# Kernel tuning notes

Measured on AMD Instinct MI355X. Metric: run time of the kernel, lower is better.

## Reference

```python
import jax, jax.numpy as jnp
import numpy as np
from jax import lax

B, H, W = 16, 96, 320
NUM_JOINTS = 9
THRESH = 0.1


def _nms(heat):
    # 3x3 max-pool NMS: keep only local maxima
    hmax = lax.reduce_window(heat, -jnp.inf, lax.max, (1, 1, 3, 3), (1, 1, 1, 1), 'SAME')
    return jnp.where(hmax == heat, heat, jnp.zeros_like(heat))


def _gather_feat(feat_bhc, ind):
    # feat_bhc: (B, HW, C), ind: (B, K) -> (B, K, C)
    return jnp.take_along_axis(feat_bhc, ind[:, :, None], axis=1)


def _transpose_and_gather_feat(feat, ind):
    # feat: (B, C, H, W), ind: (B, K) -> (B, K, C)
    b, c = feat.shape[0], feat.shape[1]
    f = feat.reshape(b, c, -1).transpose(0, 2, 1)  # (B, HW, C)
    return _gather_feat(f, ind)


def _topk(heat, K):
    b, c, h, w = heat.shape
    scores = heat.reshape(b, c, h * w)
    topk_scores, topk_inds = lax.top_k(scores, K)            # (B, C, K)
    topk_ys = (topk_inds // w).astype(heat.dtype)
    topk_xs = (topk_inds % w).astype(heat.dtype)
    topk_score, topk_ind = lax.top_k(topk_scores.reshape(b, c * K), K)  # (B, K)
    clses = topk_ind // K
    g = lambda a: jnp.take_along_axis(a.reshape(b, c * K), topk_ind, axis=1)
    return topk_score, g(topk_inds), clses, g(topk_ys), g(topk_xs)


def _topk_channel(heat, K):
    b, c, h, w = heat.shape
    scores = heat.reshape(b, c, h * w)
    topk_scores, topk_inds = lax.top_k(scores, K)  # (B, C, K)
    topk_ys = (topk_inds // w).astype(heat.dtype)
    topk_xs = (topk_inds % w).astype(heat.dtype)
    return topk_scores, topk_inds, topk_ys, topk_xs


def setup_inputs() -> dict:
    key = jax.random.key(0)
    ks = jax.random.split(key, 9)
    mk = lambda k, c: jax.random.normal(k, (B, c, H, W), dtype=jnp.float32)
    return {
        'hm': mk(ks[0], 3), 'wh': mk(ks[1], 2), 'hps': mk(ks[2], 18),
        'dim': mk(ks[3], 3), 'rot': mk(ks[4], 8), 'prob': mk(ks[5], 1),
        'reg': mk(ks[6], 2), 'hm_hp': mk(ks[7], 9), 'hp_offset': mk(ks[8], 2),
        'K': 100,
    }


def _decode(hm, wh, hps, dim, rot, prob, reg, hm_hp, hp_offset, K):
    b = hm.shape[0]
    J = hps.shape[1] // 2
    heat = _nms(jax.nn.sigmoid(hm))
    scores, inds, clses, ys0, xs0 = _topk(heat, K)  # (B, K) each

    kps = _transpose_and_gather_feat(hps, inds).reshape(b, K, J, 2)
    kps = kps + jnp.stack([xs0, ys0], axis=-1)[:, :, None, :]  # add center coords

    reg_g = _transpose_and_gather_feat(reg, inds)  # (B, K, 2)
    xs = xs0[:, :, None] + reg_g[:, :, 0:1]
    ys = ys0[:, :, None] + reg_g[:, :, 1:2]

    wh_g = _transpose_and_gather_feat(wh, inds)  # (B, K, 2)
    clses_f = clses.astype(hm.dtype)[:, :, None]
    scores_f = scores[:, :, None]
    bboxes = jnp.concatenate([xs - wh_g[..., 0:1] / 2, ys - wh_g[..., 1:2] / 2,
                              xs + wh_g[..., 0:1] / 2, ys + wh_g[..., 1:2] / 2], axis=2)

    dim_g = _transpose_and_gather_feat(dim, inds)        # (B, K, 3)
    rot_g = _transpose_and_gather_feat(rot, inds)        # (B, K, 8)
    prob_g = _transpose_and_gather_feat(prob, inds)[:, :, 0:1]  # (B, K, 1)

    # keypoint heatmap refinement
    hmhp = _nms(jax.nn.sigmoid(hm_hp))
    kps_jk = kps.transpose(0, 2, 1, 3)  # (B, J, K, 2)
    hm_score, hm_inds, hm_ys, hm_xs = _topk_channel(hmhp, K)  # (B, J, K)
    hp_off = _transpose_and_gather_feat(hp_offset, hm_inds.reshape(b, -1)).reshape(b, J, K, 2)
    hm_xs = hm_xs + hp_off[..., 0]
    hm_ys = hm_ys + hp_off[..., 1]

    valid = hm_score > THRESH
    hm_score = jnp.where(valid, hm_score, -1.0)
    hm_ys = jnp.where(valid, hm_ys, -10000.0)
    hm_xs = jnp.where(valid, hm_xs, -10000.0)
    hm_kps = jnp.stack([hm_xs, hm_ys], axis=-1)  # (B, J, K, 2)

    dist = jnp.sqrt(((kps_jk[:, :, :, None, :] - hm_kps[:, :, None, :, :]) ** 2).sum(-1))  # (B,J,K,K)
    min_dist = dist.min(axis=3)
    min_ind = dist.argmin(axis=3)  # (B, J, K)
    hm_score_sel = jnp.take_along_axis(hm_score, min_ind, axis=2)[..., None]  # (B,J,K,1)
    hm_kps_sel = jnp.take_along_axis(hm_kps, min_ind[..., None], axis=2)      # (B,J,K,2)

    l = bboxes[:, :, 0][:, None, :, None]
    t = bboxes[:, :, 1][:, None, :, None]
    r = bboxes[:, :, 2][:, None, :, None]
    bb = bboxes[:, :, 3][:, None, :, None]
    md = min_dist[..., None]
    invalid = ((hm_kps_sel[..., 0:1] < l) | (hm_kps_sel[..., 0:1] > r) |
               (hm_kps_sel[..., 1:2] < t) | (hm_kps_sel[..., 1:2] > bb) |
               (hm_score_sel < THRESH) | (md > jnp.maximum(bb - t, r - l) * 0.3))
    kps_out = jnp.where(invalid, kps_jk, hm_kps_sel)  # (B, J, K, 2)
    kps_final = kps_out.transpose(0, 2, 1, 3).reshape(b, K, J * 2) * 4.0
    hm_score_out = hm_score_sel[..., 0].transpose(0, 2, 1)  # (B, K, J)

    bboxes = bboxes * 4.0
    detections = jnp.concatenate(
        [bboxes, scores_f, kps_final, dim_g, hm_score_out, rot_g, prob_g, clses_f], axis=2)
    return detections  # (B, K, 4+1+18+3+9+8+1+1 = 45)


def reference(hm, wh, hps, dim, rot, prob, reg, hm_hp, hp_offset, K):
    return _decode(hm, wh, hps, dim, rot, prob, reg, hm_hp, hp_offset, K)
```

## Files before the change

### kernel.cpp

```cpp
#include <hip/hip_runtime.h>
#include <math.h>

typedef unsigned int u32;
typedef unsigned long long u64;

#define HW    30720
#define W_    320
#define H_    96
#define B_    16
#define KTOP  100
#define NIMG  192
#define NTHR  1024
#define SCAP  4096

__global__ __launch_bounds__(NTHR) void fused_nms_select_kernel(
    const float* __restrict__ hm, const float* __restrict__ hm_hp,
    u32* __restrict__ tkKey, u32* __restrict__ tkIdx)
{
    const int row = blockIdx.x;
    const int tid = threadIdx.x;

    __shared__ __align__(16) float img[HW];
    __shared__ u32 cidx[SCAP];
    __shared__ u32 chunkv[256];
    __shared__ u32 sel[2];
    __shared__ u32 selb2;
    __shared__ u32 cnt, cnt2;

    u64* imgU64 = (u64*)img;
    u64* cand2  = imgU64 + SCAP;
    u32* hist   = cidx;

    if (tid == 0) { cnt = 0; cnt2 = 0; }

    const float4* src4 = (const float4*)((row < 48)
        ? (hm + (size_t)row * HW) : (hm_hp + (size_t)(row - 48) * HW));
    float4* img4 = (float4*)img;
    #pragma unroll
    for (int j = 0; j < HW / 4 / NTHR + 1; ++j) {
        int i = tid + j * NTHR;
        if (i < HW / 4) img4[i] = src4[i];
    }
    __syncthreads();

    for (int q = tid; q < HW / 4; q += NTHR) {
        int pix0 = q * 4;
        int y = pix0 / W_;
        int x0 = pix0 - y * W_;
        int ym = (y > 0 ? y - 1 : 0) * W_;
        int yc = y * W_;
        int yp = (y < H_ - 1 ? y + 1 : H_ - 1) * W_;
        float cm[6];
        #pragma unroll
        for (int c = 0; c < 6; ++c) {
            int xc = x0 - 1 + c;
            xc = (xc < 0) ? 0 : (xc > W_ - 1 ? W_ - 1 : xc);
            cm[c] = fmaxf(fmaxf(img[ym + xc], img[yc + xc]), img[yp + xc]);
        }
        #pragma unroll
        for (int j = 0; j < 4; ++j) {
            float cen = img[yc + x0 + j];
            float m = fmaxf(fmaxf(cm[j], cm[j + 1]), cm[j + 2]);
            if (cen == m) {
                u32 p = atomicAdd(&cnt, 1u);
                if (p < SCAP) cidx[p] = (u32)(pix0 + j);
            }
        }
    }
    __syncthreads();

    u32 n = cnt; if (n > SCAP) n = SCAP;

    u64 kv[4];
    #pragma unroll
    for (int j = 0; j < 4; ++j) {
        u32 i = tid + j * NTHR;
        if (i < n) {
            u32 pix = cidx[i];
            float c = img[pix];
            float s = 1.0f / (1.0f + expf(-c));
            kv[j] = ((u64)__float_as_uint(s) << 32) | (u32)(~pix);
        } else kv[j] = 0ull;
    }
    __syncthreads();
    #pragma unroll
    for (int j = 0; j < 4; ++j) {
        u32 i = tid + j * NTHR;
        if (i < n) imgU64[i] = kv[j];
    }
    for (int i = tid; i < 4096; i += NTHR) hist[i] = 0;
    __syncthreads();

    for (u32 i = tid; i < n; i += NTHR)
        atomicAdd(&hist[(u32)(imgU64[i] >> 52)], 1u);
    __syncthreads();
    if (tid < 256) {
        u32 s = 0; int c0 = tid * 16;
        #pragma unroll
        for (int q = 0; q < 16; ++q) s += hist[c0 + q];
        chunkv[tid] = s;
    }
    __syncthreads();
    for (int d = 1; d < 256; d <<= 1) {
        u32 t = 0;
        if (tid < 256 - d) t = chunkv[tid + d];
        __syncthreads();
        if (tid < 256) chunkv[tid] += t;
        __syncthreads();
    }
    if (tid < 256) {
        u32 Sc = chunkv[tid];
        u32 Sn = (tid == 255) ? 0u : chunkv[tid + 1];
        if (Sc >= KTOP && Sn < KTOP) {
            u32 run = Sn, b1 = 0, G1 = 0;
            for (int bin = tid * 16 + 15; bin >= tid * 16; --bin) {
                u32 h = hist[bin];
                if (run + h >= KTOP) { b1 = (u32)bin; G1 = run; break; }
                run += h;
            }
            sel[0] = b1; sel[1] = G1;
        }
    }
    __syncthreads();
    const u32 b1 = sel[0], G1 = sel[1];

    for (int i = tid; i < 4096; i += NTHR) hist[i] = 0;
    __syncthreads();
    for (u32 i = tid; i < n; i += NTHR) {
        u32 k = (u32)(imgU64[i] >> 32);
        if ((k >> 20) == b1) atomicAdd(&hist[(k >> 8) & 0xFFFu], 1u);
    }
    __syncthreads();
    if (tid < 256) {
        u32 s = 0; int c0 = tid * 16;
        #pragma unroll
        for (int q = 0; q < 16; ++q) s += hist[c0 + q];
        chunkv[tid] = s;
    }
    __syncthreads();
    for (int d = 1; d < 256; d <<= 1) {
        u32 t = 0;
        if (tid < 256 - d) t = chunkv[tid + d];
        __syncthreads();
        if (tid < 256) chunkv[tid] += t;
        __syncthreads();
    }
    {
        const u32 K2 = KTOP - G1;
        if (tid < 256) {
            u32 Sc = chunkv[tid];
            u32 Sn = (tid == 255) ? 0u : chunkv[tid + 1];
            if (Sc >= K2 && Sn < K2) {
                u32 run = Sn, b2 = 0;
                for (int bin = tid * 16 + 15; bin >= tid * 16; --bin) {
                    u32 h = hist[bin];
                    if (run + h >= K2) { b2 = (u32)bin; break; }
                    run += h;
                }
                selb2 = b2;
            }
        }
    }
    __syncthreads();
    const u32 cut24 = (b1 << 12) | selb2;

    for (u32 i = tid; i < n; i += NTHR) {
        u64 v = imgU64[i];
        if ((u32)(v >> 40) >= cut24) {
            u32 p = atomicAdd(&cnt2, 1u);
            if (p < 2048) cand2[p] = v;
        }
    }
    __syncthreads();
    u32 m = cnt2; if (m > 2048) m = 2048;
    u32 npow = 128; while (npow < m) npow <<= 1;
    for (u32 i = m + tid; i < npow; i += NTHR) cand2[i] = 0ull;
    __syncthreads();

    for (u32 ks = 2; ks <= npow; ks <<= 1) {
        for (u32 j = ks >> 1; j > 0; j >>= 1) {
            for (u32 i = tid; i < npow; i += NTHR) {
                u32 ix = i ^ j;
                if (ix > i) {
                    u64 a = cand2[i], b = cand2[ix];
                    bool sw = ((i & ks) == 0) ? (a < b) : (a > b);
                    if (sw) { cand2[i] = b; cand2[ix] = a; }
                }
            }
            __syncthreads();
        }
    }
    if (tid < KTOP) {
        u64 v = cand2[tid];
        tkKey[row * KTOP + tid] = (u32)(v >> 32);
        tkIdx[row * KTOP + tid] = ~(u32)v;
    }
}

__global__ __launch_bounds__(256) void decode_kernel(
    const u32* __restrict__ tkKey, const u32* __restrict__ tkIdx,
    const float* __restrict__ wh,   const float* __restrict__ hps,
    const float* __restrict__ dimp, const float* __restrict__ rot,
    const float* __restrict__ prob, const float* __restrict__ reg,
    const float* __restrict__ hpo,  float* __restrict__ det)
{
    const int b = blockIdx.x;
    const int tid = threadIdx.x;

    __shared__ u64 arr[512];
    __shared__ float la[KTOP], ta[KTOP], ra[KTOP], ba2[KTOP];
    __shared__ float kx[9][KTOP], ky[9][KTOP];
    __shared__ float hsv[9][KTOP], hxv[9][KTOP], hyv[9][KTOP];

    for (int i = tid; i < 512; i += 256) {
        u64 v = 0ull;
        if (i < 300) {
            int c = i / 100, r = i - c * 100;
            u32 key = tkKey[(b * 3 + c) * KTOP + r];
            v = ((u64)key << 32) | (u32)(~(u32)i);
        }
        arr[i] = v;
    }
    __syncthreads();
    for (u32 ks = 2; ks <= 512; ks <<= 1) {
        for (u32 j = ks >> 1; j > 0; j >>= 1) {
            for (u32 i = tid; i < 512; i += 256) {
                u32 ix = i ^ j;
                if (ix > i) {
                    u64 a = arr[i], bb = arr[ix];
                    bool sw = ((i & ks) == 0) ? (a < bb) : (a > bb);
                    if (sw) { arr[i] = bb; arr[ix] = a; }
                }
            }
            __syncthreads();
        }
    }

    for (int t2 = tid; t2 < 900; t2 += 256) {
        int j = t2 / 100, r = t2 - j * 100;
        int row = 48 + b * 9 + j;
        u32 key = tkKey[row * KTOP + r];
        u32 idx = tkIdx[row * KTOP + r];
        if (idx > HW - 1) idx = HW - 1;
        float s = __uint_as_float(key);
        int yy = (int)idx / W_, xx = (int)idx - yy * W_;
        float hx = (float)xx + hpo[((size_t)b * 2 + 0) * HW + idx];
        float hy = (float)yy + hpo[((size_t)b * 2 + 1) * HW + idx];
        bool valid = s > 0.1f;
        hsv[j][r] = valid ? s : -1.0f;
        hxv[j][r] = valid ? hx : -10000.0f;
        hyv[j][r] = valid ? hy : -10000.0f;
    }

    if (tid < KTOP) {
        int k = tid;
        u64 v = arr[k];
        u32 pos = ~(u32)v;
        if (pos > 299u) pos = 299u;
        u32 key = (u32)(v >> 32);
        int c = (int)pos / 100, r = (int)pos - c * 100;
        u32 sid = tkIdx[(b * 3 + c) * KTOP + r];
        if (sid > HW - 1) sid = HW - 1;
        float score = __uint_as_float(key);
        int yy = (int)sid / W_, xx = (int)sid - yy * W_;
        float xs0 = (float)xx, ys0 = (float)yy;
        float r0 = reg[((size_t)b * 2 + 0) * HW + sid];
        float r1 = reg[((size_t)b * 2 + 1) * HW + sid];
        float xsv = xs0 + r0, ysv = ys0 + r1;
        float w0 = wh[((size_t)b * 2 + 0) * HW + sid];
        float w1 = wh[((size_t)b * 2 + 1) * HW + sid];
        float l  = xsv - w0 * 0.5f;
        float t  = ysv - w1 * 0.5f;
        float rr = xsv + w0 * 0.5f;
        float bb = ysv + w1 * 0.5f;
        la[k] = l; ta[k] = t; ra[k] = rr; ba2[k] = bb;

        float* o = det + ((size_t)b * KTOP + k) * 45;
        o[0] = l * 4.0f; o[1] = t * 4.0f; o[2] = rr * 4.0f; o[3] = bb * 4.0f;
        o[4] = score;
        #pragma unroll
        for (int q = 0; q < 3; ++q)
            o[23 + q] = dimp[((size_t)b * 3 + q) * HW + sid];
        #pragma unroll
        for (int q = 0; q < 8; ++q)
            o[35 + q] = rot[((size_t)b * 8 + q) * HW + sid];
        o[43] = prob[(size_t)b * HW + sid];
        o[44] = (float)c;
        #pragma unroll
        for (int j = 0; j < 9; ++j) {
            kx[j][k] = hps[((size_t)b * 18 + 2 * j)     * HW + sid] + xs0;
            ky[j][k] = hps[((size_t)b * 18 + 2 * j + 1) * HW + sid] + ys0;
        }
    }
    __syncthreads();

    for (int p = tid; p < 900; p += 256) {
        int j = p / 100, k = p - j * 100;
        float qx = kx[j][k], qy = ky[j][k];
        float best = INFINITY; int bi = 0;
        for (int m = 0; m < 100; ++m) {
            float dx = qx - hxv[j][m];
            float dy = qy - hyv[j][m];
            float d2 = __fadd_rn(__fmul_rn(dx, dx), __fmul_rn(dy, dy));
            float d = __fsqrt_rn(d2);
            if (d < best) { best = d; bi = m; }
        }
        float ss = hsv[j][bi], hx = hxv[j][bi], hy = hyv[j][bi];
        float l = la[k], t = ta[k], rr = ra[k], bb = ba2[k];
        float th = __fmul_rn(fmaxf(__fsub_rn(bb, t), __fsub_rn(rr, l)), 0.3f);
        bool invalid = (hx < l) | (hx > rr) | (hy < t) | (hy > bb) |
                       (ss < 0.1f) | (best > th);
        float ox = invalid ? kx[j][k] : hx;
        float oy = invalid ? ky[j][k] : hy;
        float* o = det + ((size_t)b * KTOP + k) * 45;
        o[5 + 2 * j] = ox * 4.0f;
        o[6 + 2 * j] = oy * 4.0f;
        o[26 + j]    = ss;
    }
}

extern "C" void kernel_launch(void* const* d_in, const int* in_sizes, int n_in,
                              void* d_out, int out_size, void* d_ws, size_t ws_size,
                              hipStream_t stream) {
    const float* hm    = (const float*)d_in[0];
    const float* wh    = (const float*)d_in[1];
    const float* hps   = (const float*)d_in[2];
    const float* dimp  = (const float*)d_in[3];
    const float* rot   = (const float*)d_in[4];
    const float* prob  = (const float*)d_in[5];
    const float* reg   = (const float*)d_in[6];
    const float* hm_hp = (const float*)d_in[7];
    const float* hpo   = (const float*)d_in[8];
    float* det = (float*)d_out;

    u32* tkKey = (u32*)d_ws;
    u32* tkIdx = tkKey + NIMG * KTOP;

    fused_nms_select_kernel<<<NIMG, NTHR, 0, stream>>>(hm, hm_hp, tkKey, tkIdx);
    decode_kernel<<<B_, 256, 0, stream>>>(tkKey, tkIdx, wh, hps, dimp, rot,
                                          prob, reg, hpo, det);
}
```

Measured before the change: 186.5 us.

## Drop second histogram pass, rank-select candidates, and split decode per joint

The NMS kernel now computes the sigmoid inline while collecting local maxima into separate key/pixel arrays. It drops the second 12-bit histogram refinement and keeps every candidate in the threshold bin or above. When at most 1024 survive, it replaces the bitonic sort with an O(q) per-thread rank count. The decode kernel launches 144 blocks, one per batch and joint, instead of 16, and uses a 300-way rank count in place of the 512-element bitonic sort. This adds parallelism to the decode tail, at the cost of redundant per-block gathers and a larger, possibly slower, candidate set when many scores share the top bin.

```diff
diff --git a/kernel.cpp b/kernel.cpp
--- a/kernel.cpp
+++ b/kernel.cpp
@@ -2,6 +2,7 @@
 #include <math.h>
 
 typedef unsigned int u32;
+typedef unsigned short u16;
 typedef unsigned long long u64;
 
 #define HW    30720
@@ -21,15 +22,13 @@
     const int tid = threadIdx.x;
 
     __shared__ __align__(16) float img[HW];
-    __shared__ u32 cidx[SCAP];
+    __shared__ u32 candKey[SCAP];
+    __shared__ u16 candPix[SCAP];
     __shared__ u32 chunkv[256];
-    __shared__ u32 sel[2];
-    __shared__ u32 selb2;
-    __shared__ u32 cnt, cnt2;
-
-    u64* imgU64 = (u64*)img;
-    u64* cand2  = imgU64 + SCAP;
-    u32* hist   = cidx;
+    __shared__ u32 selb1, cnt, cnt2;
+
+    u32* hist  = (u32*)img;
+    u64* cand2 = (u64*)(img + 4096);
 
     if (tid == 0) { cnt = 0; cnt2 = 0; }
 
@@ -37,7 +36,7 @@
         ? (hm + (size_t)row * HW) : (hm_hp + (size_t)(row - 48) * HW));
     float4* img4 = (float4*)img;
     #pragma unroll
-    for (int j = 0; j < HW / 4 / NTHR + 1; ++j) {
+    for (int j = 0; j < 8; ++j) {
         int i = tid + j * NTHR;
         if (i < HW / 4) img4[i] = src4[i];
     }
@@ -62,37 +61,23 @@
             float cen = img[yc + x0 + j];
             float m = fmaxf(fmaxf(cm[j], cm[j + 1]), cm[j + 2]);
             if (cen == m) {
+                float s = 1.0f / (1.0f + expf(-cen));
                 u32 p = atomicAdd(&cnt, 1u);
-                if (p < SCAP) cidx[p] = (u32)(pix0 + j);
-            }
-        }
-    }
-    __syncthreads();
-
-    u32 n = cnt; if (n > SCAP) n = SCAP;
-
-    u64 kv[4];
+                if (p < SCAP) {
+                    candKey[p] = __float_as_uint(s);
+                    candPix[p] = (u16)(pix0 + j);
+                }
+            }
+        }
+    }
+    __syncthreads();
+    const u32 n = (cnt > SCAP) ? SCAP : cnt;
+
     #pragma unroll
-    for (int j = 0; j < 4; ++j) {
-        u32 i = tid + j * NTHR;
-        if (i < n) {
-            u32 pix = cidx[i];
-            float c = img[pix];
-            float s = 1.0f / (1.0f + expf(-c));
-            kv[j] = ((u64)__float_as_uint(s) << 32) | (u32)(~pix);
-        } else kv[j] = 0ull;
-    }
-    __syncthreads();
-    #pragma unroll
-    for (int j = 0; j < 4; ++j) {
-        u32 i = tid + j * NTHR;
-        if (i < n) imgU64[i] = kv[j];
-    }
-    for (int i = tid; i < 4096; i += NTHR) hist[i] = 0;
-    __syncthreads();
-
+    for (int j = 0; j < 4; ++j) hist[tid + j * NTHR] = 0;
+    __syncthreads();
     for (u32 i = tid; i < n; i += NTHR)
-        atomicAdd(&hist[(u32)(imgU64[i] >> 52)], 1u);
+        atomicAdd(&hist[candKey[i] >> 20], 1u);
     __syncthreads();
     if (tid < 256) {
         u32 s = 0; int c0 = tid * 16;
@@ -112,149 +97,97 @@
         u32 Sc = chunkv[tid];
         u32 Sn = (tid == 255) ? 0u : chunkv[tid + 1];
         if (Sc >= KTOP && Sn < KTOP) {
-            u32 run = Sn, b1 = 0, G1 = 0;
+            u32 run = Sn;
             for (int bin = tid * 16 + 15; bin >= tid * 16; --bin) {
                 u32 h = hist[bin];
-                if (run + h >= KTOP) { b1 = (u32)bin; G1 = run; break; }
+                if (run + h >= KTOP) { selb1 = (u32)bin; break; }
                 run += h;
             }
-            sel[0] = b1; sel[1] = G1;
-        }
-    }
-    __syncthreads();
-    const u32 b1 = sel[0], G1 = sel[1];
-
-    for (int i = tid; i < 4096; i += NTHR) hist[i] = 0;
-    __syncthreads();
+        }
+    }
+    __syncthreads();
+    const u32 b1 = selb1;
+
     for (u32 i = tid; i < n; i += NTHR) {
-        u32 k = (u32)(imgU64[i] >> 32);
-        if ((k >> 20) == b1) atomicAdd(&hist[(k >> 8) & 0xFFFu], 1u);
-    }
-    __syncthreads();
-    if (tid < 256) {
-        u32 s = 0; int c0 = tid * 16;
-        #pragma unroll
-        for (int q = 0; q < 16; ++q) s += hist[c0 + q];
-        chunkv[tid] = s;
-    }
-    __syncthreads();
-    for (int d = 1; d < 256; d <<= 1) {
-        u32 t = 0;
-        if (tid < 256 - d) t = chunkv[tid + d];
+        u32 k = candKey[i];
+        if ((k >> 20) >= b1) {
+            u32 p = atomicAdd(&cnt2, 1u);
+            if (p < 2048) cand2[p] = ((u64)k << 32) | (u32)(~(u32)candPix[i]);
+        }
+    }
+    __syncthreads();
+    u32 q = cnt2; if (q > 2048) q = 2048;
+
+    if (q <= NTHR) {
+        if (tid < q) {
+            u64 v = cand2[tid];
+            u32 rank = 0;
+            for (u32 i = 0; i < q; ++i) rank += (cand2[i] > v);
+            if (rank < KTOP) {
+                tkKey[row * KTOP + rank] = (u32)(v >> 32);
+                tkIdx[row * KTOP + rank] = ~(u32)v;
+            }
+        }
+    } else {
+        u32 npow = 128; while (npow < q) npow <<= 1;
+        for (u32 i = q + tid; i < npow; i += NTHR) cand2[i] = 0ull;
         __syncthreads();
-        if (tid < 256) chunkv[tid] += t;
-        __syncthreads();
-    }
-    {
-        const u32 K2 = KTOP - G1;
-        if (tid < 256) {
-            u32 Sc = chunkv[tid];
-            u32 Sn = (tid == 255) ? 0u : chunkv[tid + 1];
-            if (Sc >= K2 && Sn < K2) {
-                u32 run = Sn, b2 = 0;
-                for (int bin = tid * 16 + 15; bin >= tid * 16; --bin) {
-                    u32 h = hist[bin];
-                    if (run + h >= K2) { b2 = (u32)bin; break; }
-                    run += h;
+        for (u32 ks = 2; ks <= npow; ks <<= 1) {
+            for (u32 j = ks >> 1; j > 0; j >>= 1) {
+                for (u32 i = tid; i < npow; i += NTHR) {
+                    u32 ix = i ^ j;
+                    if (ix > i) {
+                        u64 a = cand2[i], b = cand2[ix];
+                        bool sw = ((i & ks) == 0) ? (a < b) : (a > b);
+                        if (sw) { cand2[i] = b; cand2[ix] = a; }
+                    }
                 }
-                selb2 = b2;
-            }
-        }
-    }
-    __syncthreads();
-    const u32 cut24 = (b1 << 12) | selb2;
-
-    for (u32 i = tid; i < n; i += NTHR) {
-        u64 v = imgU64[i];
-        if ((u32)(v >> 40) >= cut24) {
-            u32 p = atomicAdd(&cnt2, 1u);
-            if (p < 2048) cand2[p] = v;
-        }
-    }
-    __syncthreads();
-    u32 m = cnt2; if (m > 2048) m = 2048;
-    u32 npow = 128; while (npow < m) npow <<= 1;
-    for (u32 i = m + tid; i < npow; i += NTHR) cand2[i] = 0ull;
-    __syncthreads();
-
-    for (u32 ks = 2; ks <= npow; ks <<= 1) {
-        for (u32 j = ks >> 1; j > 0; j >>= 1) {
-            for (u32 i = tid; i < npow; i += NTHR) {
-                u32 ix = i ^ j;
-                if (ix > i) {
-                    u64 a = cand2[i], b = cand2[ix];
-                    bool sw = ((i & ks) == 0) ? (a < b) : (a > b);
-                    if (sw) { cand2[i] = b; cand2[ix] = a; }
-                }
-            }
-            __syncthreads();
-        }
-    }
-    if (tid < KTOP) {
-        u64 v = cand2[tid];
-        tkKey[row * KTOP + tid] = (u32)(v >> 32);
-        tkIdx[row * KTOP + tid] = ~(u32)v;
+                __syncthreads();
+            }
+        }
+        if (tid < KTOP) {
+            u64 v = cand2[tid];
+            tkKey[row * KTOP + tid] = (u32)(v >> 32);
+            tkIdx[row * KTOP + tid] = ~(u32)v;
+        }
     }
 }
 
-__global__ __launch_bounds__(256) void decode_kernel(
+__global__ __launch_bounds__(320) void decode_kernel(
     const u32* __restrict__ tkKey, const u32* __restrict__ tkIdx,
     const float* __restrict__ wh,   const float* __restrict__ hps,
     const float* __restrict__ dimp, const float* __restrict__ rot,
     const float* __restrict__ prob, const float* __restrict__ reg,
     const float* __restrict__ hpo,  float* __restrict__ det)
 {
-    const int b = blockIdx.x;
+    const int blk = blockIdx.x;
+    const int b = blk / 9;
+    const int j = blk - b * 9;
     const int tid = threadIdx.x;
 
-    __shared__ u64 arr[512];
-    __shared__ float la[KTOP], ta[KTOP], ra[KTOP], ba2[KTOP];
-    __shared__ float kx[9][KTOP], ky[9][KTOP];
-    __shared__ float hsv[9][KTOP], hxv[9][KTOP], hyv[9][KTOP];
-
-    for (int i = tid; i < 512; i += 256) {
-        u64 v = 0ull;
-        if (i < 300) {
-            int c = i / 100, r = i - c * 100;
-            u32 key = tkKey[(b * 3 + c) * KTOP + r];
-            v = ((u64)key << 32) | (u32)(~(u32)i);
-        }
-        arr[i] = v;
-    }
-    __syncthreads();
-    for (u32 ks = 2; ks <= 512; ks <<= 1) {
-        for (u32 j = ks >> 1; j > 0; j >>= 1) {
-            for (u32 i = tid; i < 512; i += 256) {
-                u32 ix = i ^ j;
-                if (ix > i) {
-                    u64 a = arr[i], bb = arr[ix];
-                    bool sw = ((i & ks) == 0) ? (a < bb) : (a > bb);
-                    if (sw) { arr[i] = bb; arr[ix] = a; }
-                }
-            }
-            __syncthreads();
-        }
-    }
-
-    for (int t2 = tid; t2 < 900; t2 += 256) {
-        int j = t2 / 100, r = t2 - j * 100;
-        int row = 48 + b * 9 + j;
-        u32 key = tkKey[row * KTOP + r];
-        u32 idx = tkIdx[row * KTOP + r];
-        if (idx > HW - 1) idx = HW - 1;
-        float s = __uint_as_float(key);
-        int yy = (int)idx / W_, xx = (int)idx - yy * W_;
-        float hx = (float)xx + hpo[((size_t)b * 2 + 0) * HW + idx];
-        float hy = (float)yy + hpo[((size_t)b * 2 + 1) * HW + idx];
-        bool valid = s > 0.1f;
-        hsv[j][r] = valid ? s : -1.0f;
-        hxv[j][r] = valid ? hx : -10000.0f;
-        hyv[j][r] = valid ? hy : -10000.0f;
-    }
+    __shared__ u64 arr[300];
+    __shared__ u64 selv[KTOP];
+    __shared__ float hsv[KTOP], hxv[KTOP], hyv[KTOP];
+
+    if (tid < 300) {
+        int c = tid / 100, r = tid - c * 100;
+        u32 key = tkKey[(b * 3 + c) * KTOP + r];
+        arr[tid] = ((u64)key << 32) | (u32)(~(u32)tid);
+    }
+    __syncthreads();
+    if (tid < 300) {
+        u64 v = arr[tid];
+        u32 rank = 0;
+        for (int i = 0; i < 300; ++i) rank += (arr[i] > v);
+        if (rank < KTOP) selv[rank] = v;
+    }
+    __syncthreads();
+
+    float l = 0.f, t = 0.f, rr = 0.f, bb = 0.f, kxr = 0.f, kyr = 0.f;
 
     if (tid < KTOP) {
         int k = tid;
-        u64 v = arr[k];
+        u64 v = selv[k];
         u32 pos = ~(u32)v;
         if (pos > 299u) pos = 299u;
         u32 key = (u32)(v >> 32);
@@ -269,49 +202,67 @@
         float xsv = xs0 + r0, ysv = ys0 + r1;
         float w0 = wh[((size_t)b * 2 + 0) * HW + sid];
         float w1 = wh[((size_t)b * 2 + 1) * HW + sid];
-        float l  = xsv - w0 * 0.5f;
-        float t  = ysv - w1 * 0.5f;
-        float rr = xsv + w0 * 0.5f;
-        float bb = ysv + w1 * 0.5f;
-        la[k] = l; ta[k] = t; ra[k] = rr; ba2[k] = bb;
-
+        l  = xsv - w0 * 0.5f;
+        t  = ysv - w1 * 0.5f;
+        rr = xsv + w0 * 0.5f;
+        bb = ysv + w1 * 0.5f;
+        kxr = hps[((size_t)b * 18 + 2 * j)     * HW + sid] + xs0;
+        kyr = hps[((size_t)b * 18 + 2 * j + 1) * HW + sid] + ys0;
+        if (j == 0) {
+            float* o = det + ((size_t)b * KTOP + k) * 45;
+            o[0] = l * 4.0f; o[1] = t * 4.0f; o[2] = rr * 4.0f; o[3] = bb * 4.0f;
+            o[4] = score;
+            o[44] = (float)c;
+        }
+    } else if (tid < 200) {
+        int r = tid - 100;
+        int rw = 48 + b * 9 + j;
+        u32 key = tkKey[rw * KTOP + r];
+        u32 idx = tkIdx[rw * KTOP + r];
+        if (idx > HW - 1) idx = HW - 1;
+        float s = __uint_as_float(key);
+        int yy = (int)idx / W_, xx = (int)idx - yy * W_;
+        float hx = (float)xx + hpo[((size_t)b * 2 + 0) * HW + idx];
+        float hy = (float)yy + hpo[((size_t)b * 2 + 1) * HW + idx];
+        bool valid = s > 0.1f;
+        hsv[r] = valid ? s : -1.0f;
+        hxv[r] = valid ? hx : -10000.0f;
+        hyv[r] = valid ? hy : -10000.0f;
+    } else if (tid < 300 && j == 0) {
+        int k = tid - 200;
+        u64 v = selv[k];
+        u32 pos = ~(u32)v;
+        if (pos > 299u) pos = 299u;
+        int c = (int)pos / 100, r = (int)pos - c * 100;
+        u32 sid = tkIdx[(b * 3 + c) * KTOP + r];
+        if (sid > HW - 1) sid = HW - 1;
         float* o = det + ((size_t)b * KTOP + k) * 45;
-        o[0] = l * 4.0f; o[1] = t * 4.0f; o[2] = rr * 4.0f; o[3] = bb * 4.0f;
-        o[4] = score;
-        #pragma unroll
-        for (int q = 0; q < 3; ++q)
-            o[23 + q] = dimp[((size_t)b * 3 + q) * HW + sid];
-        #pragma unroll
-        for (int q = 0; q < 8; ++q)
-            o[35 + q] = rot[((size_t)b * 8 + q) * HW + sid];
+        #pragma unroll
+        for (int qq = 0; qq < 3; ++qq)
+            o[23 + qq] = dimp[((size_t)b * 3 + qq) * HW + sid];
+        #pragma unroll
+        for (int qq = 0; qq < 8; ++qq)
+            o[35 + qq] = rot[((size_t)b * 8 + qq) * HW + sid];
         o[43] = prob[(size_t)b * HW + sid];
-        o[44] = (float)c;
-        #pragma unroll
-        for (int j = 0; j < 9; ++j) {
-            kx[j][k] = hps[((size_t)b * 18 + 2 * j)     * HW + sid] + xs0;
-            ky[j][k] = hps[((size_t)b * 18 + 2 * j + 1) * HW + sid] + ys0;
-        }
-    }
-    __syncthreads();
-
-    for (int p = tid; p < 900; p += 256) {
-        int j = p / 100, k = p - j * 100;
-        float qx = kx[j][k], qy = ky[j][k];
+    }
+    __syncthreads();
+
+    if (tid < KTOP) {
+        int k = tid;
         float best = INFINITY; int bi = 0;
         for (int m = 0; m < 100; ++m) {
-            float dx = qx - hxv[j][m];
-            float dy = qy - hyv[j][m];
+            float dx = kxr - hxv[m];
+            float dy = kyr - hyv[m];
             float d2 = __fadd_rn(__fmul_rn(dx, dx), __fmul_rn(dy, dy));
             float d = __fsqrt_rn(d2);
             if (d < best) { best = d; bi = m; }
         }
-        float ss = hsv[j][bi], hx = hxv[j][bi], hy = hyv[j][bi];
-        float l = la[k], t = ta[k], rr = ra[k], bb = ba2[k];
+        float ss = hsv[bi], hx = hxv[bi], hy = hyv[bi];
         float th = __fmul_rn(fmaxf(__fsub_rn(bb, t), __fsub_rn(rr, l)), 0.3f);
         bool invalid = (hx < l) | (hx > rr) | (hy < t) | (hy > bb) |
                        (ss < 0.1f) | (best > th);
-        float ox = invalid ? kx[j][k] : hx;
-        float oy = invalid ? ky[j][k] : hy;
+        float ox = invalid ? kxr : hx;
+        float oy = invalid ? kyr : hy;
         float* o = det + ((size_t)b * KTOP + k) * 45;
         o[5 + 2 * j] = ox * 4.0f;
         o[6 + 2 * j] = oy * 4.0f;
@@ -337,6 +288,6 @@
     u32* tkIdx = tkKey + NIMG * KTOP;
 
     fused_nms_select_kernel<<<NIMG, NTHR, 0, stream>>>(hm, hm_hp, tkKey, tkIdx);
-    decode_kernel<<<B_, 256, 0, stream>>>(tkKey, tkIdx, wh, hps, dimp, rot,
-                                          prob, reg, hpo, det);
+    decode_kernel<<<B_ * 9, 320, 0, stream>>>(tkKey, tkIdx, wh, hps, dimp, rot,
+                                              prob, reg, hpo, det);
 }
```

Measured after the change: 163.8 us. 1.14x faster.
